# Kernel tuning notes

Measured on AMD Instinct MI355X. Metric: run time of the kernel, lower is better.

## Reference

```python
import jax, jax.numpy as jnp
import numpy as np
from math import sqrt

B, S, D_MODEL = 2, 2048, 1024
H = 16
ADIM = D_MODEL // H  # 64
K_REL = 16
N_PEMB = 2 * K_REL + 1  # 33, bidirectional rel-pos vocabulary


def setup_inputs() -> dict:
    key = jax.random.key(0)
    ks = jax.random.split(key, 8)
    sc = 0.02
    return {
        "iQ": jax.random.normal(ks[0], (B, S, D_MODEL), jnp.float32),
        "iK": jax.random.normal(ks[1], (B, S, D_MODEL), jnp.float32),
        "iV": jax.random.normal(ks[2], (B, S, D_MODEL), jnp.float32),
        "Wq": jax.random.normal(ks[3], (D_MODEL, D_MODEL), jnp.float32) * sc,
        "Wk": jax.random.normal(ks[4], (D_MODEL, D_MODEL), jnp.float32) * sc,
        "Wv": jax.random.normal(ks[5], (D_MODEL, D_MODEL), jnp.float32) * sc,
        "Wo": jax.random.normal(ks[6], (D_MODEL, D_MODEL), jnp.float32) * sc,
        "rel_pemb": jax.random.normal(ks[7], (N_PEMB, ADIM), jnp.float32) * sc,
    }


def reference(iQ, iK, iV, Wq, Wk, Wv, Wo, rel_pemb):
    b, nq, _ = iQ.shape
    seql = iK.shape[1]
    # projections -> [b, h, len, d]
    q = (iQ @ Wq).reshape(b, nq, H, ADIM).transpose(0, 2, 1, 3)
    k = (iK @ Wk).reshape(b, seql, H, ADIM).transpose(0, 2, 1, 3)
    v = (iV @ Wv).reshape(b, seql, H, ADIM).transpose(0, 2, 1, 3)
    # content scores: [b, h, nq, seql]
    scores = jnp.einsum("bhqd,bhsd->bhqs", q, k)
    # relative position bias: rel[i, j] = clamp(j - i, -K, K) + K
    pos = jnp.arange(seql)
    rel = jnp.clip(pos[None, :] - pos[:, None], -K_REL, K_REL) + K_REL
    rel = rel[seql - nq:, :]  # narrow to query rows: [nq, seql]
    e = rel_pemb[rel]  # [nq, seql, d]
    scores = scores + jnp.einsum("bhqd,qsd->bhqs", q, e)
    scores = scores / sqrt(ADIM)
    attn = jax.nn.softmax(scores, axis=-1)
    ctx = jnp.einsum("bhqs,bhsd->bqhd", attn, v).reshape(b, nq, H * ADIM)
    return ctx @ Wo
```

## Files before the change

### kernel.cpp

```cpp
#include <hip/hip_runtime.h>
#include <hip/hip_bf16.h>

#define BB 2
#define S 2048
#define DM 1024
#define H 16
#define ADIM 64
#define NP 33

typedef __bf16 bf16x8 __attribute__((ext_vector_type(8)));
typedef float f32x4 __attribute__((ext_vector_type(4)));

__device__ __forceinline__ void gload16(const void* g, void* l) {
  __builtin_amdgcn_global_load_lds(
      (__attribute__((address_space(1))) void*)(g),
      (__attribute__((address_space(3))) void*)(l), 16, 0, 0);
}

__global__ __launch_bounds__(256) void wtrans(
    const float* __restrict__ W0, const float* __restrict__ W1,
    const float* __restrict__ W2, __bf16* __restrict__ T0,
    __bf16* __restrict__ T1, __bf16* __restrict__ T2) {
  const float* W; __bf16* T;
  switch (blockIdx.z) {
    case 0: W = W0; T = T0; break;
    case 1: W = W1; T = T1; break;
    default: W = W2; T = T2; break;
  }
  __shared__ __bf16 tile[64][65];
  int j = threadIdx.x & 63, i0 = threadIdx.x >> 6;
  int n0 = blockIdx.x * 64, k0 = blockIdx.y * 64;
#pragma unroll
  for (int p = 0; p < 16; ++p) {
    int i = i0 + p * 4;
    tile[i][j] = (__bf16)W[(size_t)(k0 + i) * DM + n0 + j];
  }
  __syncthreads();
#pragma unroll
  for (int p = 0; p < 16; ++p) {
    int i = i0 + p * 4;
    T[(size_t)(n0 + i) * DM + k0 + j] = tile[j][i];
  }
}

#define LDK 40
template <bool A_FP32, int BN, typename CT>
__device__ __forceinline__ void gemm_body(const void* __restrict__ Av,
                                          const __bf16* __restrict__ BT,
                                          CT* __restrict__ C, int mode,
                                          int m0, int n0) {
  constexpr int NF = BN / 32;
  constexpr int BH = BN / 16;
  __shared__ __align__(16) __bf16 As[128 * LDK];
  __shared__ __align__(16) __bf16 Bs[BN * 32];
  int t = threadIdx.x;
  int w = t >> 6, lane = t & 63, l15 = lane & 15, quad = lane >> 4;
  int wm = w >> 1, wn = w & 1;
  constexpr int LA = A_FP32 ? LDK : 32;
  f32x4 acc[4][NF] = {};
  int lr = t >> 2;
  int lk = (t & 3) * 8;
  int r4 = lane >> 2;
  int c8 = (lane & 3) * 8;
  for (int k0 = 0; k0 < DM; k0 += 32) {
    if constexpr (A_FP32) {
#pragma unroll
      for (int rr = 0; rr < 2; ++rr) {
        int row = rr * 64 + lr;
        const float* src = (const float*)Av + (size_t)(m0 + row) * DM + k0 + lk;
        float4 a0 = *(const float4*)src;
        float4 a1 = *(const float4*)(src + 4);
        bf16x8 v;
        v[0] = (__bf16)a0.x; v[1] = (__bf16)a0.y;
        v[2] = (__bf16)a0.z; v[3] = (__bf16)a0.w;
        v[4] = (__bf16)a1.x; v[5] = (__bf16)a1.y;
        v[6] = (__bf16)a1.z; v[7] = (__bf16)a1.w;
        *(bf16x8*)&As[row * LDK + lk] = v;
      }
    } else {
#pragma unroll
      for (int q = 0; q < 2; ++q) {
        int half = w * 2 + q;
        gload16((const __bf16*)Av + (size_t)(m0 + half * 16 + r4) * DM + k0 + c8,
                &As[half * 512]);
      }
    }
#pragma unroll
    for (int q = 0; q < BH / 4; ++q) {
      int half = w * (BH / 4) + q;
      gload16(&BT[(size_t)(n0 + half * 16 + r4) * DM + k0 + c8],
              &Bs[half * 512]);
    }
    __syncthreads();
    bf16x8 af[4], bfr[NF];
#pragma unroll
    for (int mi = 0; mi < 4; ++mi)
      af[mi] = *(const bf16x8*)&As[(wm * 64 + mi * 16 + l15) * LA + quad * 8];
#pragma unroll
    for (int ni = 0; ni < NF; ++ni)
      bfr[ni] =
          *(const bf16x8*)&Bs[(wn * (BN / 2) + ni * 16 + l15) * 32 + quad * 8];
#pragma unroll
    for (int mi = 0; mi < 4; ++mi)
#pragma unroll
      for (int ni = 0; ni < NF; ++ni)
        acc[mi][ni] = __builtin_amdgcn_mfma_f32_16x16x32_bf16(
            af[mi], bfr[ni], acc[mi][ni], 0, 0, 0);
    __syncthreads();
  }
#pragma unroll
  for (int mi = 0; mi < 4; ++mi)
#pragma unroll
    for (int ni = 0; ni < NF; ++ni)
#pragma unroll
      for (int r = 0; r < 4; ++r) {
        int row = m0 + wm * 64 + mi * 16 + quad * 4 + r;
        int col = n0 + wn * (BN / 2) + ni * 16 + l15;
        CT v = (CT)acc[mi][ni][r];
        if (mode == 0) {
          C[(size_t)row * DM + col] = v;
        } else {
          int b = row >> 11, s = row & (S - 1);
          int h = col >> 6, d = col & (ADIM - 1);
          if (mode == 1)
            C[((size_t)(b * H + h) * S + s) * ADIM + d] = v;
          else
            C[((size_t)(b * H + h) * ADIM + d) * S + s] = v;
        }
      }
}

__global__ __launch_bounds__(256) void proj3(
    const float* __restrict__ iQ, const float* __restrict__ iK,
    const float* __restrict__ iV, const __bf16* __restrict__ WqT,
    const __bf16* __restrict__ WkT, const __bf16* __restrict__ WvT,
    __bf16* __restrict__ Qw, __bf16* __restrict__ Kw,
    __bf16* __restrict__ Vt) {
  const float* A; const __bf16* B; __bf16* C; int mode;
  switch (blockIdx.z) {
    case 0: A = iQ; B = WqT; C = Qw; mode = 1; break;
    case 1: A = iK; B = WkT; C = Kw; mode = 1; break;
    default: A = iV; B = WvT; C = Vt; mode = 2; break;
  }
  int i2 = blockIdx.x + (blockIdx.y << 3);
  int xcd = i2 & 7, slot = i2 >> 3;
  int m0 = (xcd + ((slot >> 3) << 3)) * 128;
  int n0 = (slot & 7) * 128;
  gemm_body<true, 128, __bf16>(A, B, C, mode, m0, n0);
}

__global__ __launch_bounds__(256) void gemm_final(
    const __bf16* __restrict__ ctx, const __bf16* __restrict__ WoT,
    float* __restrict__ out) {
  int i2 = blockIdx.x + (blockIdx.y << 4);
  int xcd = i2 & 7, slot = i2 >> 3;
  int m0 = ((xcd << 2) + (slot >> 4)) * 128;
  int n0 = (slot & 15) * 64;
  gemm_body<false, 64, float>(ctx, WoT, out, 0, m0, n0);
}

#define AST 72
__global__ __launch_bounds__(256) void attn_flash(
    const __bf16* __restrict__ Qw, const __bf16* __restrict__ Kw,
    const __bf16* __restrict__ Vt, const float* __restrict__ pemb,
    __bf16* __restrict__ ctx) {
  int bh = blockIdx.y, b = bh >> 4, h = bh & 15;
  int q0 = blockIdx.x * 128;
  int t = threadIdx.x, w = t >> 6, lane = t & 63, l15 = lane & 15,
      quad = lane >> 4;
  const __bf16* Qh = Qw + (size_t)bh * S * ADIM;
  const __bf16* Kh = Kw + (size_t)bh * S * ADIM;
  const __bf16* Vh = Vt + (size_t)bh * ADIM * S;

  __shared__ __align__(16) char smem[54272];
  __bf16* Ks = (__bf16*)smem;
  __bf16* Vs = (__bf16*)(smem + 9216);
  float* pband = (float*)(smem + 18432);
  __bf16* peb = (__bf16*)smem;

  for (int i = t; i < 48 * 64; i += 256) {
    int r = i >> 6, d = i & 63;
    peb[r * AST + d] = (r < NP) ? (__bf16)pemb[i] : (__bf16)0.f;
  }

  bf16x8 qf[2][2];
#pragma unroll
  for (int g = 0; g < 2; ++g) {
    int qa = q0 + w * 32 + g * 16 + l15;
    qf[g][0] = *(const bf16x8*)&Qh[(size_t)qa * ADIM + quad * 8];
    qf[g][1] = *(const bf16x8*)&Qh[(size_t)qa * ADIM + 32 + quad * 8];
  }
  __syncthreads();

#pragma unroll
  for (int g = 0; g < 2; ++g) {
    f32x4 pc[3] = {};
#pragma unroll
    for (int ni = 0; ni < 3; ++ni) {
      bf16x8 b0 = *(const bf16x8*)&peb[(ni * 16 + l15) * AST + quad * 8];
      bf16x8 b1 = *(const bf16x8*)&peb[(ni * 16 + l15) * AST + 32 + quad * 8];
      pc[ni] =
          __builtin_amdgcn_mfma_f32_16x16x32_bf16(qf[g][0], b0, pc[ni], 0, 0, 0);
      pc[ni] =
          __builtin_amdgcn_mfma_f32_16x16x32_bf16(qf[g][1], b1, pc[ni], 0, 0, 0);
    }
#pragma unroll
    for (int ni = 0; ni < 3; ++ni)
#pragma unroll
      for (int r = 0; r < 4; ++r) {
        int col = ni * 16 + l15;
        if (col < NP)
          pband[(w * 32 + g * 16 + quad * 4 + r) * 34 + col] = pc[ni][r];
      }
  }
  __syncthreads();

  int qw0 = q0 + w * 32;
  float lsum[2][4] = {};
  f32x4 o[2][4] = {};

  const float K2 = 0.18033688011112f;
  float pK0[2][4], pK32[2][4];
#pragma unroll
  for (int g = 0; g < 2; ++g)
#pragma unroll
    for (int r = 0; r < 4; ++r) {
      int lrow = w * 32 + g * 16 + quad * 4 + r;
      pK0[g][r] = pband[lrow * 34 + 0] * K2;
      pK32[g][r] = pband[lrow * 34 + 32] * K2;
    }

  int srow = t >> 3;
  int scol = (t & 7) * 8;
  bf16x8 k0r = *(const bf16x8*)&Kh[(size_t)srow * ADIM + scol];
  bf16x8 k1r = *(const bf16x8*)&Kh[(size_t)(32 + srow) * ADIM + scol];
  bf16x8 v0r = *(const bf16x8*)&Vh[(size_t)srow * S + scol];
  bf16x8 v1r = *(const bf16x8*)&Vh[(size_t)(32 + srow) * S + scol];

  for (int s0 = 0; s0 < S; s0 += 64) {
    __syncthreads();
    *(bf16x8*)&Ks[srow * AST + scol] = k0r;
    *(bf16x8*)&Ks[(32 + srow) * AST + scol] = k1r;
    *(bf16x8*)&Vs[srow * AST + scol] = v0r;
    *(bf16x8*)&Vs[(32 + srow) * AST + scol] = v1r;
    int sn = s0 + 64;
    if (sn < S) {
      k0r = *(const bf16x8*)&Kh[(size_t)(sn + srow) * ADIM + scol];
      k1r = *(const bf16x8*)&Kh[(size_t)(sn + 32 + srow) * ADIM + scol];
      v0r = *(const bf16x8*)&Vh[(size_t)srow * S + sn + scol];
      v1r = *(const bf16x8*)&Vh[(size_t)(32 + srow) * S + sn + scol];
    }
    __syncthreads();

    f32x4 c[2][4];
#pragma unroll
    for (int j = 0; j < 4; ++j) {
      bf16x8 kb0 = *(const bf16x8*)&Ks[(j * 16 + l15) * AST + quad * 8];
      bf16x8 kb1 = *(const bf16x8*)&Ks[(j * 16 + l15) * AST + 32 + quad * 8];
#pragma unroll
      for (int g = 0; g < 2; ++g) {
        f32x4 cj = {};
        cj = __builtin_amdgcn_mfma_f32_16x16x32_bf16(qf[g][0], kb0, cj, 0, 0, 0);
        cj = __builtin_amdgcn_mfma_f32_16x16x32_bf16(qf[g][1], kb1, cj, 0, 0, 0);
        c[g][j] = cj;
      }
    }

    float pv[2][4][4];
#pragma unroll
    for (int g = 0; g < 2; ++g) {
      int qg0 = qw0 + g * 16;
      bool below = (s0 + 79 <= qg0);
      bool above = (s0 >= qg0 + 31);
      if (below || above) {
#pragma unroll
        for (int j = 0; j < 4; ++j)
#pragma unroll
          for (int r = 0; r < 4; ++r) {
            float pk = below ? pK0[g][r] : pK32[g][r];
            float e = exp2f(__builtin_fmaf(c[g][j][r], K2, pk));
            lsum[g][r] += e;
            pv[g][j][r] = e;
          }
      } else {
#pragma unroll
        for (int j = 0; j < 4; ++j)
#pragma unroll
          for (int r = 0; r < 4; ++r) {
            int qg = qg0 + quad * 4 + r;
            int sg = s0 + j * 16 + l15;
            int i0 = sg - qg;
            i0 = i0 < -16 ? -16 : (i0 > 16 ? 16 : i0);
            i0 += 16;
            int lrow = w * 32 + g * 16 + quad * 4 + r;
            float e = exp2f((c[g][j][r] + pband[lrow * 34 + i0]) * K2);
            lsum[g][r] += e;
            pv[g][j][r] = e;
          }
      }
    }

    bf16x8 pa0[2], pa1[2];
#pragma unroll
    for (int g = 0; g < 2; ++g) {
      __bf16* pb = (__bf16*)(smem + 35840 + (w * 2 + g) * 2304);
#pragma unroll
      for (int j = 0; j < 4; ++j)
#pragma unroll
        for (int r = 0; r < 4; ++r)
          pb[(quad * 4 + r) * AST + j * 16 + l15] = (__bf16)pv[g][j][r];
      pa0[g] = *(const bf16x8*)&pb[l15 * AST + quad * 8];
      pa1[g] = *(const bf16x8*)&pb[l15 * AST + 32 + quad * 8];
    }

#pragma unroll
    for (int nt = 0; nt < 4; ++nt) {
      bf16x8 vb0 = *(const bf16x8*)&Vs[(nt * 16 + l15) * AST + quad * 8];
      bf16x8 vb1 = *(const bf16x8*)&Vs[(nt * 16 + l15) * AST + 32 + quad * 8];
#pragma unroll
      for (int g = 0; g < 2; ++g) {
        o[g][nt] =
            __builtin_amdgcn_mfma_f32_16x16x32_bf16(pa0[g], vb0, o[g][nt], 0, 0, 0);
        o[g][nt] =
            __builtin_amdgcn_mfma_f32_16x16x32_bf16(pa1[g], vb1, o[g][nt], 0, 0, 0);
      }
    }
  }

#pragma unroll
  for (int g = 0; g < 2; ++g)
#pragma unroll
    for (int r = 0; r < 4; ++r) {
#pragma unroll
      for (int mm = 1; mm < 16; mm <<= 1)
        lsum[g][r] += __shfl_xor(lsum[g][r], mm, 64);
    }
#pragma unroll
  for (int g = 0; g < 2; ++g)
#pragma unroll
    for (int nt = 0; nt < 4; ++nt)
#pragma unroll
      for (int r = 0; r < 4; ++r) {
        int qg = q0 + w * 32 + g * 16 + quad * 4 + r;
        int d = nt * 16 + l15;
        ctx[(size_t)(b * S + qg) * DM + h * ADIM + d] =
            (__bf16)(o[g][nt][r] / lsum[g][r]);
      }
}

extern "C" void kernel_launch(void* const* d_in, const int* in_sizes, int n_in,
                              void* d_out, int out_size, void* d_ws,
                              size_t ws_size, hipStream_t stream) {
  bool sizes_ok =
      (n_in == 8 && in_sizes[0] == BB * S * DM && in_sizes[1] == BB * S * DM &&
       in_sizes[2] == BB * S * DM && in_sizes[3] == DM * DM &&
       in_sizes[4] == DM * DM && in_sizes[5] == DM * DM &&
       in_sizes[6] == DM * DM && in_sizes[7] == NP * ADIM &&
       out_size == BB * S * DM);
  if (!sizes_ok) return;
  if (ws_size < 33ull * 1024 * 1024) return;

  const float* iQ = (const float*)d_in[0];
  const float* iK = (const float*)d_in[1];
  const float* iV = (const float*)d_in[2];
  const float* Wq = (const float*)d_in[3];
  const float* Wk = (const float*)d_in[4];
  const float* Wv = (const float*)d_in[5];
  const float* Wo = (const float*)d_in[6];
  const float* pemb = (const float*)d_in[7];

  char* w = (char*)d_ws;
  const size_t MB = 1024 * 1024;
  __bf16* Qw  = (__bf16*)(w + 0 * MB);
  __bf16* Kw  = (__bf16*)(w + 8 * MB);
  __bf16* Vt  = (__bf16*)(w + 16 * MB);
  __bf16* ctx = (__bf16*)(w + 24 * MB);
  __bf16* WqT = (__bf16*)(w + 24 * MB);
  __bf16* WkT = (__bf16*)(w + 26 * MB);
  __bf16* WvT = (__bf16*)(w + 28 * MB);
  __bf16* WoT = (__bf16*)(w + 0 * MB);

  wtrans<<<dim3(16, 16, 3), 256, 0, stream>>>(Wq, Wk, Wv, WqT, WkT, WvT);
  proj3<<<dim3(8, 32, 3), 256, 0, stream>>>(iQ, iK, iV, WqT, WkT, WvT,
                                            Qw, Kw, Vt);
  attn_flash<<<dim3(S / 128, BB * H), 256, 0, stream>>>(Qw, Kw, Vt, pemb, ctx);
  wtrans<<<dim3(16, 16, 1), 256, 0, stream>>>(Wo, Wo, Wo, WoT, WoT, WoT);
  gemm_final<<<dim3(16, 32), 256, 0, stream>>>(ctx, WoT, (float*)d_out);
}
```

Before: 269.7 us.

## Pre-convert activations to bf16 before projections and shrink attention LDS footprint

Adds a separate kernel that converts the fp32 Q/K/V inputs to bf16 in workspace, so the projection GEMM can use its bf16-A path instead of converting fp32 on the fly. This path is only taken when the workspace holds at least 56 MB. Separately, the attention kernel stores the relative-position band in bf16 and gives each wave one reused P buffer, which cuts LDS from about 54 KB to 36 KB so more blocks can be resident per CU. The extra conversion pass costs additional memory traffic, and the bf16 band slightly reduces bias precision.

```diff
diff --git a/kernel.cpp b/kernel.cpp
--- a/kernel.cpp
+++ b/kernel.cpp
@@ -15,6 +15,27 @@
   __builtin_amdgcn_global_load_lds(
       (__attribute__((address_space(1))) void*)(g),
       (__attribute__((address_space(3))) void*)(l), 16, 0, 0);
+}
+
+__global__ __launch_bounds__(256) void tobf16(
+    const float* __restrict__ X0, const float* __restrict__ X1,
+    const float* __restrict__ X2, __bf16* __restrict__ Y0,
+    __bf16* __restrict__ Y1, __bf16* __restrict__ Y2) {
+  const float* X; __bf16* Y;
+  switch (blockIdx.z) {
+    case 0: X = X0; Y = Y0; break;
+    case 1: X = X1; Y = Y1; break;
+    default: X = X2; Y = Y2; break;
+  }
+  size_t i = ((size_t)blockIdx.x * 256 + threadIdx.x) * 8;
+  float4 a0 = *(const float4*)(X + i);
+  float4 a1 = *(const float4*)(X + i + 4);
+  bf16x8 v;
+  v[0] = (__bf16)a0.x; v[1] = (__bf16)a0.y;
+  v[2] = (__bf16)a0.z; v[3] = (__bf16)a0.w;
+  v[4] = (__bf16)a1.x; v[5] = (__bf16)a1.y;
+  v[6] = (__bf16)a1.z; v[7] = (__bf16)a1.w;
+  *(bf16x8*)(Y + i) = v;
 }
 
 __global__ __launch_bounds__(256) void wtrans(
@@ -149,6 +170,25 @@
   gemm_body<true, 128, __bf16>(A, B, C, mode, m0, n0);
 }
 
+__global__ __launch_bounds__(256) void proj3b(
+    const __bf16* __restrict__ Qb, const __bf16* __restrict__ Kb,
+    const __bf16* __restrict__ Vb, const __bf16* __restrict__ WqT,
+    const __bf16* __restrict__ WkT, const __bf16* __restrict__ WvT,
+    __bf16* __restrict__ Qw, __bf16* __restrict__ Kw,
+    __bf16* __restrict__ Vt) {
+  const __bf16* A; const __bf16* B; __bf16* C; int mode;
+  switch (blockIdx.z) {
+    case 0: A = Qb; B = WqT; C = Qw; mode = 1; break;
+    case 1: A = Kb; B = WkT; C = Kw; mode = 1; break;
+    default: A = Vb; B = WvT; C = Vt; mode = 2; break;
+  }
+  int i2 = blockIdx.x + (blockIdx.y << 3);
+  int xcd = i2 & 7, slot = i2 >> 3;
+  int m0 = (xcd + ((slot >> 3) << 3)) * 128;
+  int n0 = (slot & 7) * 128;
+  gemm_body<false, 128, __bf16>(A, B, C, mode, m0, n0);
+}
+
 __global__ __launch_bounds__(256) void gemm_final(
     const __bf16* __restrict__ ctx, const __bf16* __restrict__ WoT,
     float* __restrict__ out) {
@@ -172,10 +212,11 @@
   const __bf16* Kh = Kw + (size_t)bh * S * ADIM;
   const __bf16* Vh = Vt + (size_t)bh * ADIM * S;
 
-  __shared__ __align__(16) char smem[54272];
+  __shared__ __align__(16) char smem[36352];
   __bf16* Ks = (__bf16*)smem;
   __bf16* Vs = (__bf16*)(smem + 9216);
-  float* pband = (float*)(smem + 18432);
+  __bf16* pband = (__bf16*)(smem + 18432);
+  __bf16* pbufw = (__bf16*)(smem + 27136 + w * 2304);
   __bf16* peb = (__bf16*)smem;
 
   for (int i = t; i < 48 * 64; i += 256) {
@@ -210,7 +251,8 @@
       for (int r = 0; r < 4; ++r) {
         int col = ni * 16 + l15;
         if (col < NP)
-          pband[(w * 32 + g * 16 + quad * 4 + r) * 34 + col] = pc[ni][r];
+          pband[(w * 32 + g * 16 + quad * 4 + r) * 34 + col] =
+              (__bf16)pc[ni][r];
       }
   }
   __syncthreads();
@@ -226,8 +268,8 @@
 #pragma unroll
     for (int r = 0; r < 4; ++r) {
       int lrow = w * 32 + g * 16 + quad * 4 + r;
-      pK0[g][r] = pband[lrow * 34 + 0] * K2;
-      pK32[g][r] = pband[lrow * 34 + 32] * K2;
+      pK0[g][r] = (float)pband[lrow * 34 + 0] * K2;
+      pK32[g][r] = (float)pband[lrow * 34 + 32] * K2;
     }
 
   int srow = t >> 3;
@@ -293,7 +335,8 @@
             i0 = i0 < -16 ? -16 : (i0 > 16 ? 16 : i0);
             i0 += 16;
             int lrow = w * 32 + g * 16 + quad * 4 + r;
-            float e = exp2f((c[g][j][r] + pband[lrow * 34 + i0]) * K2);
+            float e =
+                exp2f((c[g][j][r] + (float)pband[lrow * 34 + i0]) * K2);
             lsum[g][r] += e;
             pv[g][j][r] = e;
           }
@@ -303,14 +346,13 @@
     bf16x8 pa0[2], pa1[2];
 #pragma unroll
     for (int g = 0; g < 2; ++g) {
-      __bf16* pb = (__bf16*)(smem + 35840 + (w * 2 + g) * 2304);
 #pragma unroll
       for (int j = 0; j < 4; ++j)
 #pragma unroll
         for (int r = 0; r < 4; ++r)
-          pb[(quad * 4 + r) * AST + j * 16 + l15] = (__bf16)pv[g][j][r];
-      pa0[g] = *(const bf16x8*)&pb[l15 * AST + quad * 8];
-      pa1[g] = *(const bf16x8*)&pb[l15 * AST + 32 + quad * 8];
+          pbufw[(quad * 4 + r) * AST + j * 16 + l15] = (__bf16)pv[g][j][r];
+      pa0[g] = *(const bf16x8*)&pbufw[l15 * AST + quad * 8];
+      pa1[g] = *(const bf16x8*)&pbufw[l15 * AST + 32 + quad * 8];
     }
 
 #pragma unroll
@@ -381,8 +423,17 @@
   __bf16* WoT = (__bf16*)(w + 0 * MB);
 
   wtrans<<<dim3(16, 16, 3), 256, 0, stream>>>(Wq, Wk, Wv, WqT, WkT, WvT);
-  proj3<<<dim3(8, 32, 3), 256, 0, stream>>>(iQ, iK, iV, WqT, WkT, WvT,
-                                            Qw, Kw, Vt);
+  if (ws_size >= 56ull * 1024 * 1024) {
+    __bf16* Qb = (__bf16*)(w + 32 * MB);
+    __bf16* Kb = (__bf16*)(w + 40 * MB);
+    __bf16* Vb = (__bf16*)(w + 48 * MB);
+    tobf16<<<dim3(2048, 1, 3), 256, 0, stream>>>(iQ, iK, iV, Qb, Kb, Vb);
+    proj3b<<<dim3(8, 32, 3), 256, 0, stream>>>(Qb, Kb, Vb, WqT, WkT, WvT,
+                                               Qw, Kw, Vt);
+  } else {
+    proj3<<<dim3(8, 32, 3), 256, 0, stream>>>(iQ, iK, iV, WqT, WkT, WvT,
+                                              Qw, Kw, Vt);
+  }
   attn_flash<<<dim3(S / 128, BB * H), 256, 0, stream>>>(Qw, Kw, Vt, pemb, ctx);
   wtrans<<<dim3(16, 16, 1), 256, 0, stream>>>(Wo, Wo, Wo, WoT, WoT, WoT);
   gemm_final<<<dim3(16, 32), 256, 0, stream>>>(ctx, WoT, (float*)d_out);
```

New measurement: 261.1 us. 3.2% less time.
